# Kernel optimization log

Hardware: AMD Instinct MI355X
Metric: run time of the kernel (lower is better)

The kernel has to match this reference:

```python
import jax, jax.numpy as jnp
import numpy as np
import math
from jax import lax

B, CIN, H, W = 2, 3, 80, 80
C = 128  # out_channel
LN_EPS = 1e-5
BN_EPS = 1e-5


def _layernorm(x, g, b):
    m = x.mean(-1, keepdims=True)
    v = ((x - m) ** 2).mean(-1, keepdims=True)
    return (x - m) / jnp.sqrt(v + LN_EPS) * g + b


def _pos_enc_2d(c, h, w, dtype):
    # PositionalEncodingPermute2D: returns (c,h,w) encoding
    ch = int(np.ceil(c / 2))
    inv_freq = jnp.asarray(1.0 / (10000.0 ** (np.arange(0, ch, 2, dtype=np.float32) / ch)))
    sx = jnp.arange(h, dtype=dtype)[:, None] * inv_freq  # (h, ch//2)
    sy = jnp.arange(w, dtype=dtype)[:, None] * inv_freq  # (w, ch//2)
    emb_x = jnp.concatenate([jnp.sin(sx), jnp.cos(sx)], -1)  # (h, ch)
    emb_y = jnp.concatenate([jnp.sin(sy), jnp.cos(sy)], -1)  # (w, ch)
    emb = jnp.concatenate([
        jnp.broadcast_to(emb_x[:, None, :], (h, w, ch)),
        jnp.broadcast_to(emb_y[None, :, :], (h, w, ch)),
    ], -1)  # (h, w, 2*ch)
    return emb[:, :, :c].transpose(2, 0, 1)  # (c, h, w)


def setup_inputs() -> dict:
    key = jax.random.key(0)
    ks = jax.random.split(key, 8)
    d = {
        'x': jax.random.normal(ks[0], (B, CIN, 3, H, W), jnp.float32),
        'conv0_w': jax.random.normal(ks[1], (C, CIN * 3, 5, 5), jnp.float32) * 0.05,
        'bn_g': jnp.ones((C,), jnp.float32),
        'bn_b': jnp.zeros((C,), jnp.float32),
        'ln1_g': jnp.ones((C,), jnp.float32),
        'ln1_b': jnp.zeros((C,), jnp.float32),
        'wq': jax.random.normal(ks[2], (C, C), jnp.float32) / math.sqrt(C),
        'wk': jax.random.normal(ks[3], (C, C), jnp.float32) / math.sqrt(C),
        'wv': jax.random.normal(ks[4], (C, C), jnp.float32) / math.sqrt(C),
        'ln2_g': jnp.ones((C,), jnp.float32),
        'ln2_b': jnp.zeros((C,), jnp.float32),
        'fc1_w': jax.random.normal(ks[5], (C, 2 * C), jnp.float32) * 0.05,
        'fc1_b': jnp.zeros((2 * C,), jnp.float32),
        'fc2_w': jax.random.normal(ks[6], (2 * C, C), jnp.float32) * 0.05,
        'fc2_b': jnp.zeros((C,), jnp.float32),
    }
    return d


def reference(x, conv0_w, bn_g, bn_b, ln1_g, ln1_b, wq, wk, wv, ln2_g, ln2_b,
              fc1_w, fc1_b, fc2_w, fc2_b):
    Bn, Ci, three, Hh, Ww = x.shape
    # chunk along dim 2 and concat along channels: [lh, hh, hl]
    contact = x.transpose(0, 2, 1, 3, 4).reshape(Bn, three * Ci, Hh, Ww)
    y = lax.conv_general_dilated(contact, conv0_w, (1, 1), ((2, 2), (2, 2)),
                                 dimension_numbers=('NCHW', 'OIHW', 'NCHW'))
    # BatchNorm in eval mode: running_mean=0, running_var=1
    y = y / jnp.sqrt(1.0 + BN_EPS) * bn_g[None, :, None, None] + bn_b[None, :, None, None]
    y = jnp.where(y > 0, y, 0.2 * y)  # LeakyReLU(0.2)
    b, c, h, w = y.shape
    pe = _pos_enc_2d(c, h, w, y.dtype)
    inp = y + pe[None]
    depth = 1
    for _ in range(depth):
        t = inp.reshape(b, c, h * w).transpose(0, 2, 1)  # [b, N, c]
        qkv = _layernorm(t, ln1_g, ln1_b)
        Q = qkv @ wq
        K = qkv @ wk
        V = qkv @ wv
        scores = jnp.einsum('bnc,bmc->bnm', Q, K) / math.sqrt(c)
        A = jax.nn.softmax(scores, axis=1)  # nn.Softmax(dim=1): over first token axis
        attn = t + jnp.einsum('bnm,bmc->bnc', A, V)  # drop_path = identity (eval)
        hid = _layernorm(attn, ln2_g, ln2_b)
        m = jax.nn.gelu(hid @ fc1_w + fc1_b, approximate=False)
        m = m @ fc2_w + fc2_b
        t = attn + m
        inp = t.transpose(0, 2, 1).reshape(b, c, h, w)
    return inp
```

## Files before the change

### kernel.cpp

```cpp
#include <hip/hip_runtime.h>
#include <hip/hip_bf16.h>
#include <math.h>

typedef unsigned int u32;
typedef unsigned short u16;
typedef __attribute__((ext_vector_type(4))) float f32x4;
typedef __attribute__((ext_vector_type(8))) short bf16x8;

#define DEV __device__ __forceinline__

DEV u16 f2bf(float f) {
  union { float f; u32 u; } v; v.f = f;
  u32 u = v.u;
  return (u16)((u + 0x7FFFu + ((u >> 16) & 1u)) >> 16);
}

DEV float bf2f(u16 h) {
  union { u32 u; float f; } v; v.u = (u32)h << 16;
  return v.f;
}

DEV u32 pk2(float a, float b) {
  u32 r;
  asm("v_cvt_pk_bf16_f32 %0, %1, %2" : "=v"(r) : "v"(a), "v"(b));
  return r;
}

__global__ __launch_bounds__(256) void k_conv(
    const float* __restrict__ x, const float* __restrict__ cw,
    const float* __restrict__ bng, const float* __restrict__ bnb,
    float* __restrict__ t0, float* __restrict__ attn)
{
  __shared__ float sinp[9 * 400];
  __shared__ float sw[225 * 16];
  const int t = threadIdx.x;
  const int tile = blockIdx.x, cg = blockIdx.y, b = blockIdx.z;
  const int ty0 = (tile / 5) * 16, tx0 = (tile % 5) * 16;

  for (int i = t; i < 3600; i += 256) {
    int ci = i / 400, rem = i % 400, r = rem / 20, cc = rem % 20;
    int gy = ty0 + r - 2, gx = tx0 + cc - 2;
    float v = 0.f;
    if ((unsigned)gy < 80u && (unsigned)gx < 80u) {
      int c = ci % 3, tt = ci / 3;
      v = x[(((size_t)b * 3 + c) * 3 + tt) * 6400 + gy * 80 + gx];
    }
    sinp[i] = v;
  }
  for (int i = t; i < 3600; i += 256) {
    int c = i & 15, j = i >> 4;
    sw[i] = cw[(size_t)(cg * 16 + c) * 225 + j];
  }
  __syncthreads();

  const int lx = t & 15, ly = t >> 4;
  float acc[16];
#pragma unroll
  for (int c = 0; c < 16; c++) acc[c] = 0.f;

  for (int ci = 0; ci < 9; ci++) {
#pragma unroll
    for (int ky = 0; ky < 5; ky++) {
      const float* ro = &sinp[ci * 400 + (ly + ky) * 20 + lx];
#pragma unroll
      for (int kx = 0; kx < 5; kx++) {
        float v = ro[kx];
        const float4* w4 = (const float4*)&sw[(ci * 25 + ky * 5 + kx) * 16];
        float4 w0 = w4[0], w1 = w4[1], w2 = w4[2], w3 = w4[3];
        acc[0] += v * w0.x;  acc[1] += v * w0.y;  acc[2] += v * w0.z;  acc[3] += v * w0.w;
        acc[4] += v * w1.x;  acc[5] += v * w1.y;  acc[6] += v * w1.z;  acc[7] += v * w1.w;
        acc[8] += v * w2.x;  acc[9] += v * w2.y;  acc[10] += v * w2.z; acc[11] += v * w2.w;
        acc[12] += v * w3.x; acc[13] += v * w3.y; acc[14] += v * w3.z; acc[15] += v * w3.w;
      }
    }
  }

  const int gy = ty0 + ly, gx = tx0 + lx;
  const int n = gy * 80 + gx;
  const float rb = rsqrtf(1.f + 1e-5f);
  const float NEG_L = -logf(10000.f) / 32.f;
  float outv[16];
#pragma unroll
  for (int c = 0; c < 16; c++) {
    int co = cg * 16 + c;
    float v = acc[c] * rb * bng[co] + bnb[co];
    v = v > 0.f ? v : 0.2f * v;
    int j = (co < 64) ? co : co - 64;
    float pos = (co < 64) ? (float)gy : (float)gx;
    int k = j & 31;
    float ang = pos * __expf((float)k * NEG_L);
    v += (j < 32) ? __sinf(ang) : __cosf(ang);
    outv[c] = v;
  }
  const size_t base = ((size_t)b * 6400 + n) * 128 + cg * 16;
  float4* dst = (float4*)&t0[base];
  float4* dst2 = (float4*)&attn[base];
  const float4* src = (const float4*)outv;
  dst[0] = src[0]; dst[1] = src[1]; dst[2] = src[2]; dst[3] = src[3];
  dst2[0] = src[0]; dst2[1] = src[1]; dst2[2] = src[2]; dst2[3] = src[3];
}

__global__ __launch_bounds__(256) void k_ln(
    const float* __restrict__ X, const float* __restrict__ g,
    const float* __restrict__ bta, u16* __restrict__ O)
{
  const int w = threadIdx.x >> 6, l = threadIdx.x & 63;
  const int tok = blockIdx.x * 4 + w;
  const float2 v = ((const float2*)(X + (size_t)tok * 128))[l];
  float s = v.x + v.y;
#pragma unroll
  for (int m = 1; m < 64; m <<= 1) s += __shfl_xor(s, m);
  const float mean = s * (1.f / 128.f);
  const float dx = v.x - mean, dy = v.y - mean;
  float q = dx * dx + dy * dy;
#pragma unroll
  for (int m = 1; m < 64; m <<= 1) q += __shfl_xor(q, m);
  const float rstd = rsqrtf(q * (1.f / 128.f) + 1e-5f);
  const float2 gg = ((const float2*)g)[l];
  const float2 bb = ((const float2*)bta)[l];
  const float o0 = dx * rstd * gg.x + bb.x;
  const float o1 = dy * rstd * gg.y + bb.y;
  ((u32*)O)[(size_t)tok * 64 + l] = (u32)f2bf(o0) | ((u32)f2bf(o1) << 16);
}

__global__ __launch_bounds__(256) void k_wconv_qkv(
    const float* __restrict__ wq, const float* __restrict__ wk,
    const float* __restrict__ wv, u16* __restrict__ o)
{
  const int z = blockIdx.y;
  const float* in = (z == 0) ? wq : (z == 1) ? wk : wv;
  u16* out = o + (size_t)z * 16384;
  const int i = blockIdx.x * 256 + threadIdx.x;
  const int n = i & 127, k = i >> 7;
  out[n * 128 + k] = f2bf(in[i]);
}

__global__ __launch_bounds__(256) void k_wt(
    const float* __restrict__ in, u16* __restrict__ out, int K, int N)
{
  const int i = blockIdx.x * 256 + threadIdx.x;
  if (i >= K * N) return;
  const int n = i % N, k = i / N;
  out[n * K + k] = f2bf(in[i]);
}

template <int KDIM, int NTILE, int EPI>
DEV void gemm_body(const u16* __restrict__ A, const u16* __restrict__ WT,
                   void* __restrict__ OUT, const float* __restrict__ bias,
                   const float* __restrict__ res, float scale, int bm)
{
  constexpr int PS = KDIM * 2 + 16;
  constexpr int KSTEPS = KDIM / 32;
  constexpr int CF = NTILE / 64;
  constexpr int CPR = KDIM * 2 / 16;
  __shared__ alignas(16) char As[64 * PS];
  __shared__ alignas(16) char Ws[NTILE * PS];
  const int t = threadIdx.x;
  {
    const uint4* g = (const uint4*)(A + (size_t)bm * 64 * KDIM);
    for (int i = t; i < 64 * CPR; i += 256) {
      int r = i / CPR, s = i - r * CPR;
      *(uint4*)(As + r * PS + s * 16) = g[i];
    }
    const uint4* gw = (const uint4*)WT;
    for (int i = t; i < NTILE * CPR; i += 256) {
      int r = i / CPR, s = i - r * CPR;
      *(uint4*)(Ws + r * PS + s * 16) = gw[i];
    }
  }
  __syncthreads();
  const int w = t >> 6, l = t & 63, lr = l & 15, lg = l >> 4;
  const int col0 = w * (NTILE / 4);
  f32x4 acc[4][CF] = {};
#pragma unroll
  for (int ks = 0; ks < KSTEPS; ks++) {
    const int koff = ks * 64 + lg * 16;
    bf16x8 a[4], bfr[CF];
#pragma unroll
    for (int rf = 0; rf < 4; rf++)
      a[rf] = *(const bf16x8*)(As + (rf * 16 + lr) * PS + koff);
#pragma unroll
    for (int cf = 0; cf < CF; cf++)
      bfr[cf] = *(const bf16x8*)(Ws + (col0 + cf * 16 + lr) * PS + koff);
#pragma unroll
    for (int rf = 0; rf < 4; rf++)
#pragma unroll
      for (int cf = 0; cf < CF; cf++)
        acc[rf][cf] = __builtin_amdgcn_mfma_f32_16x16x32_bf16(a[rf], bfr[cf], acc[rf][cf], 0, 0, 0);
  }
#pragma unroll
  for (int rf = 0; rf < 4; rf++) {
#pragma unroll
    for (int cf = 0; cf < CF; cf++) {
#pragma unroll
      for (int r = 0; r < 4; r++) {
        const int row = bm * 64 + rf * 16 + lg * 4 + r;
        const int col = col0 + cf * 16 + lr;
        float v = acc[rf][cf][r] * scale;
        if (EPI == 0) {
          ((u16*)OUT)[(size_t)row * NTILE + col] = f2bf(v);
        } else if (EPI == 1) {
          v += bias[col];
          v = 0.5f * v * (1.f + erff(v * 0.70710678118654752f));
          ((u16*)OUT)[(size_t)row * NTILE + col] = f2bf(v);
        } else {
          v += bias[col] + res[(size_t)row * NTILE + col];
          ((float*)OUT)[(size_t)row * NTILE + col] = v;
        }
      }
    }
  }
}

__global__ __launch_bounds__(256) void k_qkv(
    const u16* __restrict__ A, const u16* __restrict__ wT,
    u16* __restrict__ Q, u16* __restrict__ K, u16* __restrict__ V, float qscale)
{
  const int z = blockIdx.y;
  const u16* wt = wT + (size_t)z * 16384;
  u16* o = (z == 0) ? Q : (z == 1) ? K : V;
  gemm_body<128, 128, 0>(A, wt, o, nullptr, nullptr, (z == 0) ? qscale : 1.0f, blockIdx.x);
}

__global__ __launch_bounds__(256) void k_fc1(
    const u16* __restrict__ A, const u16* __restrict__ wt,
    u16* __restrict__ o, const float* __restrict__ bias)
{
  gemm_body<128, 256, 1>(A, wt, o, bias, nullptr, 1.f, blockIdx.x);
}

__global__ __launch_bounds__(256) void k_fc2(
    const u16* __restrict__ A, const u16* __restrict__ wt,
    float* __restrict__ o, const float* __restrict__ bias, const float* __restrict__ res)
{
  gemm_body<256, 128, 2>(A, wt, o, bias, res, 1.f, blockIdx.x);
}

__global__ __launch_bounds__(256) void k_trv(
    const u16* __restrict__ in, const float* __restrict__ csum, u16* __restrict__ out)
{
  __shared__ u16 tile[32][33];
  const int b = blockIdx.z;
  const int r0 = blockIdx.x * 32, c0 = blockIdx.y * 32;
  const u16* ib = in + (size_t)b * 819200;
  u16* ob = out + (size_t)b * 819200;
  const int lx = threadIdx.x & 31, ly = threadIdx.x >> 5;
#pragma unroll
  for (int i = 0; i < 4; i++) {
    int r = ly + i * 8;
    tile[r][lx] = ib[(size_t)(r0 + r) * 128 + (c0 + lx)];
  }
  __syncthreads();
  const float rcs = 1.f / csum[(size_t)b * 6400 + r0 + lx];
#pragma unroll
  for (int i = 0; i < 4; i++) {
    int r = ly + i * 8;
    ob[(size_t)(c0 + r) * 6400 + (r0 + lx)] = f2bf(bf2f(tile[lx][r]) * rcs);
  }
}

__global__ __launch_bounds__(256) void k_tr_f32(const float* __restrict__ in, float* __restrict__ out)
{
  __shared__ float tile[32][33];
  const int b = blockIdx.z;
  const int r0 = blockIdx.x * 32, c0 = blockIdx.y * 32;
  const float* ib = in + (size_t)b * 819200;
  float* ob = out + (size_t)b * 819200;
  const int lx = threadIdx.x & 31, ly = threadIdx.x >> 5;
#pragma unroll
  for (int i = 0; i < 4; i++) {
    int r = ly + i * 8;
    tile[r][lx] = ib[(size_t)(r0 + r) * 128 + c0 + lx];
  }
  __syncthreads();
#pragma unroll
  for (int i = 0; i < 4; i++) {
    int r = ly + i * 8;
    ob[(size_t)(c0 + r) * 6400 + r0 + lx] = tile[lx][r];
  }
}

__global__ __launch_bounds__(256) void k_phasea(
    const u16* __restrict__ Qb, const u16* __restrict__ Kb, float* __restrict__ colsum)
{
  constexpr int PS = 272;
  __shared__ alignas(16) char sK[128 * PS];
  __shared__ alignas(16) char sQ[64 * PS];
  const int t = threadIdx.x;
  const int mb = blockIdx.x, split = blockIdx.y, b = blockIdx.z;
  {
    const uint4* g = (const uint4*)(Kb + ((size_t)b * 6400 + mb * 128) * 128);
    for (int i = t; i < 128 * 16; i += 256) {
      int r = i >> 4, s = i & 15;
      *(uint4*)(sK + r * PS + s * 16) = g[i];
    }
  }
  const int w = t >> 6, l = t & 63, lr = l & 15, lg = l >> 4;
  const int col0 = w * 32;
  const int tile0 = split * 6 + (split < 4 ? split : 4);
  const int ntile = 6 + (split < 4 ? 1 : 0);
  float cs0 = 0.f, cs1 = 0.f;
  for (int tt = 0; tt < ntile; tt++) {
    __syncthreads();
    {
      const uint4* g = (const uint4*)(Qb + ((size_t)b * 6400 + (tile0 + tt) * 64) * 128);
      for (int i = t; i < 64 * 16; i += 256) {
        int r = i >> 4, s = i & 15;
        *(uint4*)(sQ + r * PS + s * 16) = g[i];
      }
    }
    __syncthreads();
    f32x4 acc[4][2] = {};
#pragma unroll
    for (int ks = 0; ks < 4; ks++) {
      const int koff = ks * 64 + lg * 16;
      bf16x8 a[4], bb[2];
#pragma unroll
      for (int rf = 0; rf < 4; rf++)
        a[rf] = *(const bf16x8*)(sQ + (rf * 16 + lr) * PS + koff);
#pragma unroll
      for (int cf = 0; cf < 2; cf++)
        bb[cf] = *(const bf16x8*)(sK + (col0 + cf * 16 + lr) * PS + koff);
#pragma unroll
      for (int rf = 0; rf < 4; rf++)
#pragma unroll
        for (int cf = 0; cf < 2; cf++)
          acc[rf][cf] = __builtin_amdgcn_mfma_f32_16x16x32_bf16(a[rf], bb[cf], acc[rf][cf], 0, 0, 0);
    }
#pragma unroll
    for (int rf = 0; rf < 4; rf++)
#pragma unroll
      for (int r = 0; r < 4; r++) {
        cs0 += __builtin_amdgcn_exp2f(acc[rf][0][r]);
        cs1 += __builtin_amdgcn_exp2f(acc[rf][1][r]);
      }
  }
  cs0 += __shfl_xor(cs0, 16); cs0 += __shfl_xor(cs0, 32);
  cs1 += __shfl_xor(cs1, 16); cs1 += __shfl_xor(cs1, 32);
  if (l < 16) {
    float* base = colsum + (size_t)b * 6400 + mb * 128 + col0;
    atomicAdd(base + l, cs0);
    atomicAdd(base + 16 + l, cs1);
  }
}

__global__ __launch_bounds__(256) void k_phaseb(
    const u16* __restrict__ Qb, const u16* __restrict__ Kb, const u16* __restrict__ Vt,
    float* __restrict__ attn)
{
  constexpr int PP = 144;
  __shared__ alignas(16) char sP[2][64 * PP];
  const int t = threadIdx.x;
  const int nb = blockIdx.x, split = blockIdx.y, b = blockIdx.z;
  const int w = t >> 6, l = t & 63, lr = l & 15, lg = l >> 4;

  bf16x8 qreg[4][4];
  {
    const u16* Qrow = Qb + ((size_t)b * 6400 + nb * 64) * 128;
#pragma unroll
    for (int cf = 0; cf < 4; cf++)
#pragma unroll
      for (int ks = 0; ks < 4; ks++)
        qreg[cf][ks] = *(const bf16x8*)(Qrow + (size_t)(cf * 16 + lr) * 128 + ks * 32 + lg * 8);
  }

  const u16* Kbb = Kb + (size_t)b * 819200;
  const u16* Vtb = Vt + (size_t)b * 819200;
  f32x4 apv[4][2] = {};
  const int mt0 = (split * 100) / 8, mt1 = ((split + 1) * 100) / 8;
  int p = 0;
  for (int mt = mt0; mt < mt1; mt++) {
    const int m0 = mt * 64;
    bf16x8 vreg[2][2];
#pragma unroll
    for (int cf = 0; cf < 2; cf++)
#pragma unroll
      for (int ks = 0; ks < 2; ks++)
        vreg[cf][ks] = *(const bf16x8*)(Vtb + (size_t)(w * 32 + cf * 16 + lr) * 6400 + m0 + ks * 32 + lg * 8);

    f32x4 as[4] = {};
#pragma unroll
    for (int ks = 0; ks < 4; ks++) {
      bf16x8 af = *(const bf16x8*)(Kbb + (size_t)(m0 + w * 16 + lr) * 128 + ks * 32 + lg * 8);
#pragma unroll
      for (int cf = 0; cf < 4; cf++)
        as[cf] = __builtin_amdgcn_mfma_f32_16x16x32_bf16(af, qreg[cf][ks], as[cf], 0, 0, 0);
    }
    char* sPp = sP[p];
#pragma unroll
    for (int cf = 0; cf < 4; cf++) {
      u32 p0 = pk2(__builtin_amdgcn_exp2f(as[cf][0]), __builtin_amdgcn_exp2f(as[cf][1]));
      u32 p1 = pk2(__builtin_amdgcn_exp2f(as[cf][2]), __builtin_amdgcn_exp2f(as[cf][3]));
      *(uint2*)(sPp + (cf * 16 + lr) * PP + (w * 16 + lg * 4) * 2) = make_uint2(p0, p1);
    }
    __syncthreads();
#pragma unroll
    for (int ks = 0; ks < 2; ks++) {
#pragma unroll
      for (int nf = 0; nf < 4; nf++) {
        bf16x8 av = *(const bf16x8*)(sPp + (nf * 16 + lr) * PP + ks * 64 + lg * 16);
#pragma unroll
        for (int cf = 0; cf < 2; cf++)
          apv[nf][cf] = __builtin_amdgcn_mfma_f32_16x16x32_bf16(av, vreg[cf][ks], apv[nf][cf], 0, 0, 0);
      }
    }
    p ^= 1;
  }
  float* ab = attn + (size_t)b * 6400 * 128;
#pragma unroll
  for (int nf = 0; nf < 4; nf++)
#pragma unroll
    for (int cf = 0; cf < 2; cf++)
#pragma unroll
      for (int r = 0; r < 4; r++) {
        const int row = nb * 64 + nf * 16 + lg * 4 + r;
        const int col = w * 32 + cf * 16 + lr;
        atomicAdd(&ab[(size_t)row * 128 + col], apv[nf][cf][r]);
      }
}

extern "C" void kernel_launch(void* const* d_in, const int* in_sizes, int n_in,
                              void* d_out, int out_size, void* d_ws, size_t ws_size,
                              hipStream_t stream)
{
  (void)in_sizes; (void)n_in; (void)out_size; (void)ws_size;
  const float* x      = (const float*)d_in[0];
  const float* conv0w = (const float*)d_in[1];
  const float* bn_g   = (const float*)d_in[2];
  const float* bn_b   = (const float*)d_in[3];
  const float* ln1_g  = (const float*)d_in[4];
  const float* ln1_b  = (const float*)d_in[5];
  const float* wq     = (const float*)d_in[6];
  const float* wk     = (const float*)d_in[7];
  const float* wv     = (const float*)d_in[8];
  const float* ln2_g  = (const float*)d_in[9];
  const float* ln2_b  = (const float*)d_in[10];
  const float* fc1_w  = (const float*)d_in[11];
  const float* fc1_b  = (const float*)d_in[12];
  const float* fc2_w  = (const float*)d_in[13];
  const float* fc2_b  = (const float*)d_in[14];

  char* ws = (char*)d_ws;
  size_t off = 0;
  auto alloc = [&](size_t sz) -> void* {
    void* p = ws + off;
    off = (off + sz + 255) & ~(size_t)255;
    return p;
  };
  float* t0   = (float*)alloc((size_t)2 * 6400 * 128 * 4);
  u16* ln1o   = (u16*)alloc((size_t)2 * 6400 * 128 * 2);
  u16* Qb     = (u16*)alloc((size_t)2 * 6400 * 128 * 2);
  u16* Kb     = (u16*)alloc((size_t)2 * 6400 * 128 * 2);
  u16* Vb     = (u16*)alloc((size_t)2 * 6400 * 128 * 2);
  u16* Vtb    = (u16*)alloc((size_t)2 * 6400 * 128 * 2);
  float* csum = (float*)alloc((size_t)2 * 6400 * 4);
  float* attn = (float*)alloc((size_t)2 * 6400 * 128 * 4);
  u16* m1     = (u16*)alloc((size_t)2 * 6400 * 256 * 2);
  u16* wT     = (u16*)alloc((size_t)3 * 128 * 128 * 2);
  u16* fc1t   = (u16*)alloc((size_t)256 * 128 * 2);
  u16* fc2t   = (u16*)alloc((size_t)128 * 256 * 2);

  const float qscale = (float)(1.4426950408889634 * 0.08838834764831845);

  hipMemsetAsync(csum, 0, (size_t)2 * 6400 * 4, stream);
  k_wconv_qkv<<<dim3(64, 3, 1), 256, 0, stream>>>(wq, wk, wv, wT);
  k_wt<<<128, 256, 0, stream>>>(fc1_w, fc1t, 128, 256);
  k_wt<<<128, 256, 0, stream>>>(fc2_w, fc2t, 256, 128);
  k_conv<<<dim3(25, 8, 2), 256, 0, stream>>>(x, conv0w, bn_g, bn_b, t0, attn);
  k_ln<<<3200, 256, 0, stream>>>(t0, ln1_g, ln1_b, ln1o);
  k_qkv<<<dim3(200, 3, 1), 256, 0, stream>>>(ln1o, wT, Qb, Kb, Vb, qscale);
  k_phasea<<<dim3(50, 16, 2), 256, 0, stream>>>(Qb, Kb, csum);
  k_trv<<<dim3(200, 4, 2), 256, 0, stream>>>(Vb, csum, Vtb);
  k_phaseb<<<dim3(100, 8, 2), 256, 0, stream>>>(Qb, Kb, Vtb, attn);
  k_ln<<<3200, 256, 0, stream>>>(attn, ln2_g, ln2_b, ln1o);
  k_fc1<<<200, 256, 0, stream>>>(ln1o, fc1t, m1, fc1_b);
  k_fc2<<<200, 256, 0, stream>>>(m1, fc2t, t0, fc2_b, attn);
  k_tr_f32<<<dim3(200, 4, 2), 256, 0, stream>>>(t0, (float*)d_out);
}
```

Before: 252.1 us.

## Materialize exp scores in phase A and replace recompute with P·V GEMM

Phase A now writes the exponentiated attention scores to a large bf16 workspace matrix P (2×6400×6400). A new k_pv kernel then multiplies P by the transposed, normalized V, replacing phase B, which recomputed QK^T and the exponentials. This trades the second score computation for about 160 MB of scattered 2-byte global writes plus a re-read of P. The path only runs if the workspace is large enough, otherwise it falls back to the old kernel.

```diff
diff --git a/kernel.cpp b/kernel.cpp
--- a/kernel.cpp
+++ b/kernel.cpp
@@ -281,7 +281,8 @@
 }
 
 __global__ __launch_bounds__(256) void k_phasea(
-    const u16* __restrict__ Qb, const u16* __restrict__ Kb, float* __restrict__ colsum)
+    const u16* __restrict__ Qb, const u16* __restrict__ Kb, float* __restrict__ colsum,
+    u16* __restrict__ P)
 {
   constexpr int PS = 272;
   __shared__ alignas(16) char sK[128 * PS];
@@ -299,6 +300,7 @@
   const int col0 = w * 32;
   const int tile0 = split * 6 + (split < 4 ? split : 4);
   const int ntile = 6 + (split < 4 ? 1 : 0);
+  u16* Pbb = P ? (P + (size_t)b * 40960000) : nullptr;
   float cs0 = 0.f, cs1 = 0.f;
   for (int tt = 0; tt < ntile; tt++) {
     __syncthreads();
@@ -327,13 +329,23 @@
         for (int cf = 0; cf < 2; cf++)
           acc[rf][cf] = __builtin_amdgcn_mfma_f32_16x16x32_bf16(a[rf], bb[cf], acc[rf][cf], 0, 0, 0);
     }
-#pragma unroll
-    for (int rf = 0; rf < 4; rf++)
-#pragma unroll
-      for (int r = 0; r < 4; r++) {
-        cs0 += __builtin_amdgcn_exp2f(acc[rf][0][r]);
-        cs1 += __builtin_amdgcn_exp2f(acc[rf][1][r]);
-      }
+    const int nbase = (tile0 + tt) * 64;
+#pragma unroll
+    for (int rf = 0; rf < 4; rf++) {
+#pragma unroll
+      for (int cf = 0; cf < 2; cf++) {
+#pragma unroll
+        for (int r = 0; r < 4; r++) {
+          float e = __builtin_amdgcn_exp2f(acc[rf][cf][r]);
+          if (Pbb) {
+            const int n = nbase + rf * 16 + lg * 4 + r;
+            const int m = mb * 128 + col0 + cf * 16 + lr;
+            Pbb[(size_t)n * 6400 + m] = f2bf(e);
+          }
+          if (cf == 0) cs0 += e; else cs1 += e;
+        }
+      }
+    }
   }
   cs0 += __shfl_xor(cs0, 16); cs0 += __shfl_xor(cs0, 32);
   cs1 += __shfl_xor(cs1, 16); cs1 += __shfl_xor(cs1, 32);
@@ -342,6 +354,60 @@
     atomicAdd(base + l, cs0);
     atomicAdd(base + 16 + l, cs1);
   }
+}
+
+__global__ __launch_bounds__(256) void k_pv(
+    const u16* __restrict__ P, const u16* __restrict__ Vt, float* __restrict__ attn)
+{
+  constexpr int PR = 144;
+  __shared__ alignas(16) char As[64 * PR];
+  __shared__ alignas(16) char Bs[128 * PR];
+  const int t = threadIdx.x;
+  const int nb = blockIdx.x, split = blockIdx.y, b = blockIdx.z;
+  const int w = t >> 6, l = t & 63, lr = l & 15, lg = l >> 4;
+  const u16* Pb = P + (size_t)b * 40960000 + (size_t)(nb * 64) * 6400;
+  const u16* Vtb = Vt + (size_t)b * 819200;
+  f32x4 acc[4][2] = {};
+  for (int it = 0; it < 25; it++) {
+    const int m0 = (split * 25 + it) * 64;
+    __syncthreads();
+    for (int i = t; i < 512; i += 256) {
+      int r = i >> 3, s = i & 7;
+      *(uint4*)(As + r * PR + s * 16) = *(const uint4*)(Pb + (size_t)r * 6400 + m0 + s * 8);
+    }
+    for (int i = t; i < 1024; i += 256) {
+      int r = i >> 3, s = i & 7;
+      *(uint4*)(Bs + r * PR + s * 16) = *(const uint4*)(Vtb + (size_t)r * 6400 + m0 + s * 8);
+    }
+    __syncthreads();
+#pragma unroll
+    for (int ks = 0; ks < 2; ks++) {
+      const int koff = ks * 64 + lg * 16;
+      bf16x8 av[4], bv[2];
+#pragma unroll
+      for (int nf = 0; nf < 4; nf++)
+        av[nf] = *(const bf16x8*)(As + (nf * 16 + lr) * PR + koff);
+#pragma unroll
+      for (int cf = 0; cf < 2; cf++)
+        bv[cf] = *(const bf16x8*)(Bs + (w * 32 + cf * 16 + lr) * PR + koff);
+#pragma unroll
+      for (int nf = 0; nf < 4; nf++)
+#pragma unroll
+        for (int cf = 0; cf < 2; cf++)
+          acc[nf][cf] = __builtin_amdgcn_mfma_f32_16x16x32_bf16(av[nf], bv[cf], acc[nf][cf], 0, 0, 0);
+    }
+  }
+  float* ab = attn + (size_t)b * 819200;
+#pragma unroll
+  for (int nf = 0; nf < 4; nf++)
+#pragma unroll
+    for (int cf = 0; cf < 2; cf++)
+#pragma unroll
+      for (int r = 0; r < 4; r++) {
+        const int row = nb * 64 + nf * 16 + lg * 4 + r;
+        const int col = w * 32 + cf * 16 + lr;
+        atomicAdd(&ab[(size_t)row * 128 + col], acc[nf][cf][r]);
+      }
 }
 
 __global__ __launch_bounds__(256) void k_phaseb(
@@ -423,7 +489,7 @@
                               void* d_out, int out_size, void* d_ws, size_t ws_size,
                               hipStream_t stream)
 {
-  (void)in_sizes; (void)n_in; (void)out_size; (void)ws_size;
+  (void)in_sizes; (void)n_in; (void)out_size;
   const float* x      = (const float*)d_in[0];
   const float* conv0w = (const float*)d_in[1];
   const float* bn_g   = (const float*)d_in[2];
@@ -459,6 +525,8 @@
   u16* wT     = (u16*)alloc((size_t)3 * 128 * 128 * 2);
   u16* fc1t   = (u16*)alloc((size_t)256 * 128 * 2);
   u16* fc2t   = (u16*)alloc((size_t)128 * 256 * 2);
+  u16* P      = (u16*)alloc((size_t)2 * 6400 * 6400 * 2);
+  const bool useP = (off <= ws_size);
 
   const float qscale = (float)(1.4426950408889634 * 0.08838834764831845);
 
@@ -469,9 +537,12 @@
   k_conv<<<dim3(25, 8, 2), 256, 0, stream>>>(x, conv0w, bn_g, bn_b, t0, attn);
   k_ln<<<3200, 256, 0, stream>>>(t0, ln1_g, ln1_b, ln1o);
   k_qkv<<<dim3(200, 3, 1), 256, 0, stream>>>(ln1o, wT, Qb, Kb, Vb, qscale);
-  k_phasea<<<dim3(50, 16, 2), 256, 0, stream>>>(Qb, Kb, csum);
+  k_phasea<<<dim3(50, 16, 2), 256, 0, stream>>>(Qb, Kb, csum, useP ? P : nullptr);
   k_trv<<<dim3(200, 4, 2), 256, 0, stream>>>(Vb, csum, Vtb);
-  k_phaseb<<<dim3(100, 8, 2), 256, 0, stream>>>(Qb, Kb, Vtb, attn);
+  if (useP)
+    k_pv<<<dim3(100, 4, 2), 256, 0, stream>>>(P, Vtb, attn);
+  else
+    k_phaseb<<<dim3(100, 8, 2), 256, 0, stream>>>(Qb, Kb, Vtb, attn);
   k_ln<<<3200, 256, 0, stream>>>(attn, ln2_g, ln2_b, ln1o);
   k_fc1<<<200, 256, 0, stream>>>(ln1o, fc1t, m1, fc1_b);
   k_fc2<<<200, 256, 0, stream>>>(m1, fc2t, t0, fc2_b, attn);
```

New measurement: 233.8 us. 7.2% less time.
